# Kernel tuning notes

Measured on AMD Instinct MI355X. Metric: run time of the kernel, lower is better.

The kernel has to match this reference:

```python
import jax, jax.numpy as jnp
import numpy as np

# Multi-scale feature pyramid (static: determines per-level slice bounds)
SPATIAL_SHAPES = np.array([[100, 100], [50, 50], [25, 25], [13, 13], [7, 7]])  # (H, W) per level
LEVEL_START = np.concatenate([[0], np.cumsum(SPATIAL_SHAPES[:, 0] * SPATIAL_SHAPES[:, 1])])[:-1]
C = 256       # hidden_inplanes
HEADS = 8     # head_nums
POINTS = 4    # point_nums
LEVELS = 5    # feature_level_nums
FF = 2048     # feedforward_planes
DH = C // HEADS


def setup_inputs() -> dict:
    key = jax.random.key(0)
    ks = jax.random.split(key, 16)
    B = 2
    L = int((SPATIAL_SHAPES[:, 0] * SPATIAL_SHAPES[:, 1]).sum())  # 13343 tokens
    s = 0.02
    return {
        'src': jax.random.normal(ks[0], (B, L, C), jnp.float32),
        'pos': jax.random.normal(ks[1], (B, L, C), jnp.float32) * 0.1,
        'reference_points': jax.random.uniform(ks[2], (B, L, LEVELS, 2), jnp.float32),
        'wv': jax.random.normal(ks[3], (C, C), jnp.float32) * s,
        'bv': jnp.zeros((C,), jnp.float32),
        'wo': jax.random.normal(ks[4], (C, HEADS * LEVELS * POINTS * 2), jnp.float32) * s,
        'bo': jax.random.normal(ks[5], (HEADS * LEVELS * POINTS * 2,), jnp.float32) * 0.5,
        'wa': jax.random.normal(ks[6], (C, HEADS * LEVELS * POINTS), jnp.float32) * s,
        'ba': jnp.zeros((HEADS * LEVELS * POINTS,), jnp.float32),
        'wout': jax.random.normal(ks[7], (C, C), jnp.float32) * s,
        'bout': jnp.zeros((C,), jnp.float32),
        'ln1g': jnp.ones((C,), jnp.float32),
        'ln1b': jnp.zeros((C,), jnp.float32),
        'w1': jax.random.normal(ks[8], (C, FF), jnp.float32) * s,
        'b1': jnp.zeros((FF,), jnp.float32),
        'w2': jax.random.normal(ks[9], (FF, C), jnp.float32) * s,
        'b2': jnp.zeros((C,), jnp.float32),
        'ln2g': jnp.ones((C,), jnp.float32),
        'ln2b': jnp.zeros((C,), jnp.float32),
    }


def layernorm(x, g, b, eps=1e-5):
    m = jnp.mean(x, -1, keepdims=True)
    v = jnp.var(x, -1, keepdims=True)
    return (x - m) * jax.lax.rsqrt(v + eps) * g + b


def bilinear_sample(val, loc, Hs, Ws):
    # val: [B, heads, H*W, dh]   loc: [B, heads, Lq, P, 2] normalized coords in [0,1]
    # grid_sample semantics, align_corners=False, zero padding outside
    px = loc[..., 0] * Ws - 0.5
    py = loc[..., 1] * Hs - 0.5
    x0 = jnp.floor(px); y0 = jnp.floor(py)
    lx = px - x0;       ly = py - y0
    x0i = x0.astype(jnp.int32); y0i = y0.astype(jnp.int32)
    gather = jax.vmap(jax.vmap(lambda v, i: v[i]))  # over batch, head dims
    out = jnp.zeros(loc.shape[:-1] + (val.shape[-1],), val.dtype)
    for dx, dy, w in ((0, 0, (1 - lx) * (1 - ly)), (1, 0, lx * (1 - ly)),
                      (0, 1, (1 - lx) * ly), (1, 1, lx * ly)):
        xi = x0i + dx; yi = y0i + dy
        valid = (xi >= 0) & (xi < Ws) & (yi >= 0) & (yi < Hs)
        idx = jnp.clip(yi, 0, Hs - 1) * Ws + jnp.clip(xi, 0, Ws - 1)
        g = gather(val, idx)  # [B, heads, Lq, P, dh]
        out = out + (w * valid)[..., None] * g
    return out


def msdeform_attn(query, value_in, ref, wv, bv, wo, bo, wa, ba, wout, bout):
    B, Lq, _ = query.shape
    # value projection -> [B, heads, Len, dh]
    value = (value_in @ wv + bv).reshape(B, -1, HEADS, DH).transpose(0, 2, 1, 3)
    offsets = (query @ wo + bo).reshape(B, Lq, HEADS, LEVELS, POINTS, 2)
    attn = jax.nn.softmax((query @ wa + ba).reshape(B, Lq, HEADS, LEVELS * POINTS), -1)
    attn = attn.reshape(B, Lq, HEADS, LEVELS, POINTS)
    # offset normalizer = (W, H) per level
    norml = jnp.asarray(SPATIAL_SHAPES[:, ::-1].copy(), jnp.float32)
    loc = ref[:, :, None, :, None, :] + offsets / norml[None, None, None, :, None, :]
    acc = jnp.zeros((B, Lq, HEADS, DH), query.dtype)
    for l in range(LEVELS):
        Hs, Ws = int(SPATIAL_SHAPES[l, 0]), int(SPATIAL_SHAPES[l, 1])
        s = int(LEVEL_START[l])
        vl = value[:, :, s:s + Hs * Ws, :]
        locl = jnp.transpose(loc[:, :, :, l], (0, 2, 1, 3, 4))  # [B, heads, Lq, P, 2]
        samp = bilinear_sample(vl, locl, Hs, Ws)                 # [B, heads, Lq, P, dh]
        acc = acc + jnp.einsum('bhqpd,bqhp->bqhd', samp, attn[:, :, :, l])
    return acc.reshape(B, Lq, C) @ wout + bout


def reference(src, pos, reference_points, wv, bv, wo, bo, wa, ba, wout, bout,
              ln1g, ln1b, w1, b1, w2, b2, ln2g, ln2b):
    # DeformableTransformerEncoderLayer (eval mode, dropout off)
    q = src + pos
    src2 = msdeform_attn(q, src, reference_points, wv, bv, wo, bo, wa, ba, wout, bout)
    x = layernorm(src + src2, ln1g, ln1b)
    ffn = jax.nn.relu(x @ w1 + b1) @ w2 + b2
    return layernorm(x + ffn, ln2g, ln2b)
```

## Files before the change

kernel.cpp:

```cpp
#include <hip/hip_runtime.h>
#include <hip/hip_bf16.h>
#include <hip/hip_fp16.h>

typedef __hip_bfloat16 bf16;
typedef unsigned short ushort_t;
typedef __attribute__((ext_vector_type(8))) short bf16x8;
typedef __attribute__((ext_vector_type(16))) float f32x16;

__device__ __forceinline__ float us2f(unsigned short u) {
    unsigned int x = ((unsigned int)u) << 16;
    return __uint_as_float(x);
}
__device__ __forceinline__ ushort_t f2us(float f) {
    return ((__hip_bfloat16_raw)__float2bfloat16(f)).x;
}

__device__ __forceinline__ void gl_lds16(const ushort_t* g, ushort_t* l) {
    __builtin_amdgcn_global_load_lds(
        (const __attribute__((address_space(1))) void*)g,
        (__attribute__((address_space(3))) void*)l, 16, 0, 0);
}

__global__ __launch_bounds__(256) void cast2_kernel(
    const float* __restrict__ src, const float* __restrict__ pos,
    bf16* __restrict__ src_b, bf16* __restrict__ q_b, int n)
{
    int i = (blockIdx.x * 256 + threadIdx.x) * 4;
    if (i < n) {
        const float4 s4 = *reinterpret_cast<const float4*>(&src[i]);
        const float4 p4 = *reinterpret_cast<const float4*>(&pos[i]);
        int2 sp, qp;
        sp.x = (unsigned)f2us(s4.x) | ((unsigned)f2us(s4.y) << 16);
        sp.y = (unsigned)f2us(s4.z) | ((unsigned)f2us(s4.w) << 16);
        qp.x = (unsigned)f2us(s4.x + p4.x) | ((unsigned)f2us(s4.y + p4.y) << 16);
        qp.y = (unsigned)f2us(s4.z + p4.z) | ((unsigned)f2us(s4.w + p4.w) << 16);
        *reinterpret_cast<int2*>((ushort_t*)src_b + i) = sp;
        *reinterpret_cast<int2*>((ushort_t*)q_b + i) = qp;
    }
}

__global__ __launch_bounds__(256) void prep_kernel(
    const float* __restrict__ wv, const float* __restrict__ wo,
    const float* __restrict__ wa, const float* __restrict__ wout,
    const float* __restrict__ w1, const float* __restrict__ w2,
    const float* __restrict__ bo, const float* __restrict__ ba,
    bf16* __restrict__ wvt, bf16* __restrict__ wcat, bf16* __restrict__ woutt,
    bf16* __restrict__ w1t, bf16* __restrict__ w2t, float* __restrict__ bcat)
{
    __shared__ float tile[32][33];
    const int b = blockIdx.x;
    const float* W; bf16* Wt; int K, N, tb;
    if (b < 64)        { W = wv;   Wt = wvt;            K = 256;  N = 256;  tb = b; }
    else if (b < 144)  { W = wo;   Wt = wcat;           K = 256;  N = 320;  tb = b - 64; }
    else if (b < 184)  { W = wa;   Wt = wcat + 320*256; K = 256;  N = 160;  tb = b - 144; }
    else if (b < 248)  { W = wout; Wt = woutt;          K = 256;  N = 256;  tb = b - 184; }
    else if (b < 760)  { W = w1;   Wt = w1t;            K = 256;  N = 2048; tb = b - 248; }
    else if (b < 1272) { W = w2;   Wt = w2t;            K = 2048; N = 256;  tb = b - 760; }
    else {
        int i = (b - 1272) * 256 + threadIdx.x;
        if (i < 320) bcat[i] = bo[i];
        else if (i < 480) bcat[i] = ba[i - 320];
        return;
    }
    const int ntn = N >> 5;
    const int nb = (tb % ntn) * 32, kb = (tb / ntn) * 32;
    const int tx = threadIdx.x & 31, ty = threadIdx.x >> 5;
    #pragma unroll
    for (int i = 0; i < 32; i += 8) {
        int k = kb + ty + i, n = nb + tx;
        tile[ty + i][tx] = (k < K && n < N) ? W[(size_t)k * N + n] : 0.f;
    }
    __syncthreads();
    #pragma unroll
    for (int i = 0; i < 32; i += 8) {
        int n = nb + ty + i, k = kb + tx;
        if (n < N && k < K)
            Wt[(size_t)n * K + k] = __float2bfloat16(tile[tx][ty + i]);
    }
}

template<bool RELU, bool OUT_BF16, bool HAS_RESID, bool RESID_BF16, int NT, int WPE>
__global__ __launch_bounds__(256, WPE) void gemm_mfma_s(
    const ushort_t* __restrict__ A,
    const ushort_t* __restrict__ Bt,
    const float* __restrict__ bias,
    const void* __restrict__ residv,
    void* __restrict__ outv, int M, int N, int K, int mtiles)
{
    __shared__ __align__(16) char smemraw[24576];
    ushort_t* Asmem = (ushort_t*)smemraw;
    ushort_t* Bsmem = (ushort_t*)(smemraw + 4096);
    float (*epi)[68] = (float(*)[68])smemraw;

    const int lid = blockIdx.x;
    const int tbk = lid >> 3;
    const int xb = tbk & (NT - 1);
    const int yg = (tbk / NT) * 8 + (lid & 7);
    if (yg >= mtiles) return;
    const int m0 = yg * 64;
    const int n0 = xb * 128;

    const int tid = threadIdx.x;
    const int lane = tid & 63;
    const int wave = tid >> 6;
    const int l32 = lane & 31;
    const int hi  = lane >> 5;
    const int wm = wave >> 1;
    const int wn = wave & 1;

    const int lsup = lane >> 3;
    const int clin = lane & 7;

    const int gsA = wave * 8 + lsup;
    const int csA = clin ^ (gsA & 7);
    int rA = m0 + gsA * 2 + (csA >> 2); if (rA > M - 1) rA = M - 1;
    const ushort_t* aP = A + (size_t)rA * K + (csA & 3) * 8;
    ushort_t* aL = Asmem + wave * 512;

    const ushort_t* bP[2]; ushort_t* bL[2];
    #pragma unroll
    for (int i = 0; i < 2; ++i) {
        const int gsB = wave * 16 + i * 8 + lsup;
        const int csB = clin ^ (gsB & 7);
        int rB = n0 + gsB * 2 + (csB >> 2); if (rB > N - 1) rB = N - 1;
        bP[i] = Bt + (size_t)rB * K + (csB & 3) * 8;
        bL[i] = Bsmem + (wave * 16 + i * 8) * 64;
    }

    const int arow = wm * 32 + l32;
    const int asup = arow >> 1;
    const ushort_t* aR[2];
    #pragma unroll
    for (int kw = 0; kw < 2; ++kw) {
        const int q = kw * 2 + hi;
        const int slot = (((arow & 1) << 2) | q) ^ (asup & 7);
        aR[kw] = Asmem + asup * 64 + slot * 8;
    }
    const ushort_t* bR[2][2];
    #pragma unroll
    for (int j = 0; j < 2; ++j) {
        const int brow = wn * 64 + j * 32 + l32;
        const int bsup = brow >> 1;
        #pragma unroll
        for (int kw = 0; kw < 2; ++kw) {
            const int q = kw * 2 + hi;
            const int slot = (((brow & 1) << 2) | q) ^ (bsup & 7);
            bR[j][kw] = Bsmem + bsup * 64 + slot * 8;
        }
    }

    f32x16 acc[2] = {};

    auto stage = [&](int ofs) {
        gl_lds16(aP, aL + ofs);             aP    += 32;
        gl_lds16(bP[0], bL[0] + ofs);       bP[0] += 32;
        gl_lds16(bP[1], bL[1] + ofs);       bP[1] += 32;
    };
    auto compute = [&](int ofs) {
        #pragma unroll
        for (int kw = 0; kw < 2; ++kw) {
            const bf16x8 af = *reinterpret_cast<const bf16x8*>(aR[kw] + ofs);
            #pragma unroll
            for (int j = 0; j < 2; ++j)
                acc[j] = __builtin_amdgcn_mfma_f32_32x32x16_bf16(
                    af, *reinterpret_cast<const bf16x8*>(bR[j][kw] + ofs),
                    acc[j], 0, 0, 0);
        }
    };

    const int ntile = K >> 5;
    stage(0);
    for (int t = 0; t < ntile; t += 2) {
        __syncthreads();
        stage(6144);
        compute(0);
        __syncthreads();
        if (t + 2 < ntile) stage(0);
        compute(6144);
    }
    __syncthreads();

    #pragma unroll
    for (int half = 0; half < 2; ++half) {
        if (wn == half) {
            #pragma unroll
            for (int j = 0; j < 2; ++j) {
                const int coll = j * 32 + l32;
                const int n = n0 + half * 64 + coll;
                const float bv = (n < N) ? bias[n] : 0.f;
                #pragma unroll
                for (int r = 0; r < 16; ++r) {
                    const int row = wm * 32 + hi * 4 + (r & 3) + (r >> 2) * 8;
                    epi[row][coll] = acc[j][r] + bv;
                }
            }
        }
        __syncthreads();
        #pragma unroll
        for (int i = 0; i < 4; ++i) {
            const int idx = i * 256 + tid;
            const int row = idx >> 4;
            const int c4  = idx & 15;
            const int m = m0 + row;
            const int n = n0 + half * 64 + c4 * 4;
            if (m < M && n + 3 < N) {
                float4 v = *reinterpret_cast<const float4*>(&epi[row][c4 * 4]);
                if (HAS_RESID) {
                    if (RESID_BF16) {
                        const int2 rw = *reinterpret_cast<const int2*>(
                            (const ushort_t*)residv + (size_t)m * N + n);
                        v.x += us2f((ushort_t)((unsigned)rw.x & 0xffffu));
                        v.y += us2f((ushort_t)((unsigned)rw.x >> 16));
                        v.z += us2f((ushort_t)((unsigned)rw.y & 0xffffu));
                        v.w += us2f((ushort_t)((unsigned)rw.y >> 16));
                    } else {
                        const float4 r4 = *reinterpret_cast<const float4*>(
                            (const float*)residv + (size_t)m * N + n);
                        v.x += r4.x; v.y += r4.y; v.z += r4.z; v.w += r4.w;
                    }
                }
                if (RELU) {
                    v.x = fmaxf(v.x, 0.f); v.y = fmaxf(v.y, 0.f);
                    v.z = fmaxf(v.z, 0.f); v.w = fmaxf(v.w, 0.f);
                }
                if (OUT_BF16) {
                    int2 pk;
                    pk.x = (unsigned)f2us(v.x) | ((unsigned)f2us(v.y) << 16);
                    pk.y = (unsigned)f2us(v.z) | ((unsigned)f2us(v.w) << 16);
                    *reinterpret_cast<int2*>((ushort_t*)outv + (size_t)m * N + n) = pk;
                } else {
                    *reinterpret_cast<float4*>((float*)outv + (size_t)m * N + n) = v;
                }
            }
        }
        if (half == 0) __syncthreads();
    }
}

__global__ __launch_bounds__(256) void msda_kernel_v7(
    const ushort_t* __restrict__ og,
    const float* __restrict__ refp,
    const ushort_t* __restrict__ value,
    bf16* __restrict__ out,
    int M, int L)
{
    const int tid = threadIdx.x;
    const int nb = gridDim.x;
    int wk = blockIdx.x;
    if ((nb & 7) == 0) {
        const int per = nb >> 3;
        wk = (blockIdx.x & 7) * per + (blockIdx.x >> 3);
    }
    const int qbase = wk * 8;

    __shared__ float s_attn[8][160];
    __shared__ int2  s_off[1280];
    __shared__ int2  s_wh[1280];

    for (int i = tid; i < 1280; i += 256) {
        int q = i / 160, j = i - q * 160;
        int qq = qbase + q;
        s_attn[q][j] = (qq < M) ? us2f(og[(size_t)qq * 480 + 320 + j]) : 0.f;
    }
    __syncthreads();

    if (tid < 64) {
        float* a = &s_attn[tid >> 3][(tid & 7) * 20];
        float mx = -1e30f;
        #pragma unroll
        for (int i = 0; i < 20; ++i) mx = fmaxf(mx, a[i]);
        float ssum = 0.f;
        #pragma unroll
        for (int i = 0; i < 20; ++i) {
            float e = __expf(a[i] - mx);
            a[i] = e;
            ssum += e;
        }
        float inv = 1.f / ssum;
        #pragma unroll
        for (int i = 0; i < 20; ++i) a[i] *= inv;
    }
    __syncthreads();

    #pragma unroll
    for (int it = 0; it < 5; ++it) {
        const int t = tid + it * 256;
        const int q  = t / 160;
        const int r  = t - q * 160;
        const int l  = (r - (r / 20) * 20) >> 2;
        const int qq = qbase + q;

        int2 offp = {0, 0};
        __half2 h01 = __floats2half2_rn(0.f, 0.f);
        __half2 h23 = h01;
        if (qq < M) {
            const int Wi = (l == 0) ? 100 : (l == 1) ? 50 : (l == 2) ? 25
                         : (l == 3) ? 13 : 7;
            const int s0 = (l == 0) ? 0 : (l == 1) ? 10000 : (l == 2) ? 12500
                         : (l == 3) ? 13125 : 13294;
            const float Wf = (float)Wi;
            const float ox = us2f(og[(size_t)qq * 480 + r * 2]);
            const float oy = us2f(og[(size_t)qq * 480 + r * 2 + 1]);
            const float2 rf = *reinterpret_cast<const float2*>(
                &refp[(size_t)qq * 10 + l * 2]);
            const float a = s_attn[q][r];

            const float px = fmaf(rf.x, Wf, -0.5f) + ox;
            const float py = fmaf(rf.y, Wf, -0.5f) + oy;
            const float x0f = floorf(px);
            const float y0f = floorf(py);
            const float lx = px - x0f;
            const float ly = py - y0f;
            const int x0 = (int)x0f;
            const int y0 = (int)y0f;

            const float wx0v = (x0 >= 0 && x0 < Wi) ? (1.f - lx) : 0.f;
            const float wx1v = (x0 + 1 >= 0 && x0 + 1 < Wi) ? lx : 0.f;
            const float wy0v = (y0 >= 0 && y0 < Wi) ? (1.f - ly) : 0.f;
            const float wy1v = (y0 + 1 >= 0 && y0 + 1 < Wi) ? ly : 0.f;

            const int c0 = min(max(x0, 0), Wi - 2);
            const int r0 = min(max(y0, 0), Wi - 2);
            const float swx0 = (x0 == c0 ? wx0v : 0.f) + (x0 + 1 == c0 ? wx1v : 0.f);
            const float swx1 = (x0 == c0 + 1 ? wx0v : 0.f) + (x0 + 1 == c0 + 1 ? wx1v : 0.f);
            const float swy0 = (y0 == r0 ? wy0v : 0.f) + (y0 + 1 == r0 ? wy1v : 0.f);
            const float swy1 = (y0 == r0 + 1 ? wy0v : 0.f) + (y0 + 1 == r0 + 1 ? wy1v : 0.f);

            offp.x = (s0 + r0 * Wi + c0) * 512;
            offp.y = offp.x + Wi * 512;
            h01 = __floats2half2_rn(a * swx0 * swy0, a * swx1 * swy0);
            h23 = __floats2half2_rn(a * swx0 * swy1, a * swx1 * swy1);
        }
        s_off[t] = offp;
        union { __half2 h; int i; } c0u, c1u;
        c0u.h = h01; c1u.h = h23;
        int2 wpk; wpk.x = c0u.i; wpk.y = c1u.i;
        s_wh[t] = wpk;
    }
    __syncthreads();

    const int qi  = tid >> 5;
    const int g   = tid & 31;
    const int h   = g >> 2;
    const int sub = g & 3;
    const int bq = qbase + qi;
    if (bq >= M) return;
    const int b = bq / L;

    const char* vb = (const char*)value + (size_t)b * L * 512 + h * 64 + sub * 16;

    float acc[8] = {};
    const int tb = qi * 160 + h * 20;
    #pragma unroll 2
    for (int p = 0; p < 20; ++p) {
        const int2 off = s_off[tb + p];
        const int2 whp = s_wh[tb + p];
        const int4 u00 = *reinterpret_cast<const int4*>(vb + off.x);
        const int4 u10 = *reinterpret_cast<const int4*>(vb + off.x + 512);
        const int4 u01 = *reinterpret_cast<const int4*>(vb + off.y);
        const int4 u11 = *reinterpret_cast<const int4*>(vb + off.y + 512);
        union { int i; __half2 h; } w0u, w1u;
        w0u.i = whp.x; w1u.i = whp.y;
        const float2 w01 = __half22float2(w0u.h);
        const float2 w23 = __half22float2(w1u.h);
        #define ACC4(u, wt)                                                        \
            acc[0] = fmaf(wt, __uint_as_float((unsigned)(u).x << 16), acc[0]);      \
            acc[1] = fmaf(wt, __uint_as_float((unsigned)(u).x & 0xffff0000u), acc[1]); \
            acc[2] = fmaf(wt, __uint_as_float((unsigned)(u).y << 16), acc[2]);      \
            acc[3] = fmaf(wt, __uint_as_float((unsigned)(u).y & 0xffff0000u), acc[3]); \
            acc[4] = fmaf(wt, __uint_as_float((unsigned)(u).z << 16), acc[4]);      \
            acc[5] = fmaf(wt, __uint_as_float((unsigned)(u).z & 0xffff0000u), acc[5]); \
            acc[6] = fmaf(wt, __uint_as_float((unsigned)(u).w << 16), acc[6]);      \
            acc[7] = fmaf(wt, __uint_as_float((unsigned)(u).w & 0xffff0000u), acc[7]);
        ACC4(u00, w01.x)
        ACC4(u10, w01.y)
        ACC4(u01, w23.x)
        ACC4(u11, w23.y)
        #undef ACC4
    }

    ushort_t o[8];
    #pragma unroll
    for (int i = 0; i < 8; ++i) o[i] = f2us(acc[i]);
    int4 pkt;
    pkt.x = (int)o[0] | ((int)o[1] << 16);
    pkt.y = (int)o[2] | ((int)o[3] << 16);
    pkt.z = (int)o[4] | ((int)o[5] << 16);
    pkt.w = (int)o[6] | ((int)o[7] << 16);
    *reinterpret_cast<int4*>((ushort_t*)out + (size_t)bq * 256 + h * 32 + sub * 8) = pkt;
}

template<bool OUT_BF16>
__global__ __launch_bounds__(256) void ln_kernel(
    const ushort_t* __restrict__ yb, const float* __restrict__ g,
    const float* __restrict__ bta, void* __restrict__ outv, int M)
{
    const int wave = threadIdx.x >> 6, lane = threadIdx.x & 63;
    const int row = blockIdx.x * 4 + wave;
    if (row >= M) return;
    const int2 raw = *reinterpret_cast<const int2*>(&yb[(size_t)row * 256 + lane * 4]);
    float v0 = us2f((ushort_t)((unsigned)raw.x & 0xffffu));
    float v1 = us2f((ushort_t)((unsigned)raw.x >> 16));
    float v2 = us2f((ushort_t)((unsigned)raw.y & 0xffffu));
    float v3 = us2f((ushort_t)((unsigned)raw.y >> 16));
    float s  = v0 + v1 + v2 + v3;
    float ss = v0 * v0 + v1 * v1 + v2 * v2 + v3 * v3;
    #pragma unroll
    for (int o = 32; o > 0; o >>= 1) {
        s += __shfl_down(s, o);
        ss += __shfl_down(ss, o);
    }
    s = __shfl(s, 0);
    ss = __shfl(ss, 0);
    const float mean = s * (1.f / 256.f);
    const float var = ss * (1.f / 256.f) - mean * mean;
    const float rs = rsqrtf(var + 1e-5f);
    const float4 g4 = *reinterpret_cast<const float4*>(&g[lane * 4]);
    const float4 b4 = *reinterpret_cast<const float4*>(&bta[lane * 4]);
    float4 o4;
    o4.x = (v0 - mean) * rs * g4.x + b4.x;
    o4.y = (v1 - mean) * rs * g4.y + b4.y;
    o4.z = (v2 - mean) * rs * g4.z + b4.z;
    o4.w = (v3 - mean) * rs * g4.w + b4.w;
    if (OUT_BF16) {
        int2 pk;
        pk.x = (unsigned)f2us(o4.x) | ((unsigned)f2us(o4.y) << 16);
        pk.y = (unsigned)f2us(o4.z) | ((unsigned)f2us(o4.w) << 16);
        *reinterpret_cast<int2*>((ushort_t*)outv + (size_t)row * 256 + lane * 4) = pk;
    } else {
        *reinterpret_cast<float4*>((float*)outv + (size_t)row * 256 + lane * 4) = o4;
    }
}

extern "C" void kernel_launch(void* const* d_in, const int* in_sizes, int n_in,
                              void* d_out, int out_size, void* d_ws, size_t ws_size,
                              hipStream_t stream)
{
    const int B = 2, L = 13343, C = 256, FF = 2048;
    const int M = B * L;

    const float* src  = (const float*)d_in[0];
    const float* pos  = (const float*)d_in[1];
    const float* refp = (const float*)d_in[2];
    const float* wv   = (const float*)d_in[3];
    const float* bv   = (const float*)d_in[4];
    const float* wo   = (const float*)d_in[5];
    const float* bo   = (const float*)d_in[6];
    const float* wa   = (const float*)d_in[7];
    const float* ba   = (const float*)d_in[8];
    const float* wout = (const float*)d_in[9];
    const float* bout = (const float*)d_in[10];
    const float* ln1g = (const float*)d_in[11];
    const float* ln1b = (const float*)d_in[12];
    const float* w1   = (const float*)d_in[13];
    const float* b1   = (const float*)d_in[14];
    const float* w2   = (const float*)d_in[15];
    const float* b2   = (const float*)d_in[16];
    const float* ln2g = (const float*)d_in[17];
    const float* ln2b = (const float*)d_in[18];

    char* ws = (char*)d_ws;
    const size_t MB = 1ull << 20;
    bf16*  src_b  = (bf16*)(ws + 0);
    bf16*  q_b    = (bf16*)(ws + 14 * MB);
    bf16*  val_b  = (bf16*)(ws + 28 * MB);
    bf16*  og     = (bf16*)(ws + 42 * MB);
    bf16*  acc_b  = (bf16*)(ws + 95 * MB);
    bf16*  h_b    = (bf16*)(ws + 0);
    bf16*  y      = (bf16*)(ws + 110 * MB);
    bf16*  z      = (bf16*)(ws + 110 * MB);
    bf16*  x_b    = (bf16*)(ws + 138 * MB);
    bf16* wvt    = (bf16*)(ws + 152 * MB);
    bf16* wcat   = wvt + 256 * 256;
    bf16* woutt  = wcat + 480 * 256;
    bf16* w1t    = woutt + 256 * 256;
    bf16* w2t    = w1t + 2048 * 256;
    float* bcat  = (float*)(w2t + 256 * 2048);
    (void)ws_size; (void)n_in; (void)in_sizes; (void)out_size;

    const int mt64 = (M + 63) / 64;
    const int gm8  = (mt64 + 7) / 8;
    const int lnb  = (M + 3) / 4;

    prep_kernel<<<1274, 256, 0, stream>>>(wv, wo, wa, wout, w1, w2, bo, ba,
                                          wvt, wcat, woutt, w1t, w2t, bcat);

    cast2_kernel<<<(M * C / 4 + 255) / 256, 256, 0, stream>>>(
        src, pos, src_b, q_b, M * C);

    gemm_mfma_s<false, true, false, false, 2, 4><<<gm8 * 16, 256, 0, stream>>>(
        (const ushort_t*)src_b, (const ushort_t*)wvt, bv, nullptr, val_b,
        M, 256, 256, mt64);

    gemm_mfma_s<false, true, false, false, 4, 4><<<gm8 * 32, 256, 0, stream>>>(
        (const ushort_t*)q_b, (const ushort_t*)wcat, bcat, nullptr, og,
        M, 480, 256, mt64);

    msda_kernel_v7<<<(M + 7) / 8, 256, 0, stream>>>(
        (const ushort_t*)og, refp, (const ushort_t*)val_b, acc_b, M, L);

    gemm_mfma_s<false, true, true, false, 2, 4><<<gm8 * 16, 256, 0, stream>>>(
        (const ushort_t*)acc_b, (const ushort_t*)woutt, bout, src, y,
        M, 256, 256, mt64);

    ln_kernel<true><<<lnb, 256, 0, stream>>>(
        (const ushort_t*)y, ln1g, ln1b, x_b, M);

    gemm_mfma_s<true, true, false, false, 16, 4><<<gm8 * 128, 256, 0, stream>>>(
        (const ushort_t*)x_b, (const ushort_t*)w1t, b1, nullptr, h_b,
        M, FF, 256, mt64);

    gemm_mfma_s<false, true, true, true, 2, 4><<<gm8 * 16, 256, 0, stream>>>(
        (const ushort_t*)h_b, (const ushort_t*)w2t, b2, x_b, z,
        M, 256, FF, mt64);

    ln_kernel<false><<<lnb, 256, 0, stream>>>(
        (const ushort_t*)z, ln2g, ln2b, (float*)d_out, M);
}
```

Measured before the change: 354.0 us.

## Add 128x128-tile MFMA GEMM and use it for projection and FFN GEMMs

Adds a new GEMM kernel with 128x128 output tiles, where each wave computes a 64x64 block from four 32x32x16 bf16 MFMAs. It double-buffers K-slices in LDS through direct global-to-LDS loads with an XOR swizzle, and writes the epilogue through an LDS staging buffer in quadrants. The offset/attention projection GEMM and both FFN GEMMs now use this kernel instead of the 64-row-tile kernel. The goal is more operand reuse per LDS load and higher arithmetic intensity. In exchange there are fewer blocks (grid tail effects), more register pressure, and extra syncs in the epilogue.

```diff
diff --git a/kernel.cpp b/kernel.cpp
--- a/kernel.cpp
+++ b/kernel.cpp
@@ -234,6 +234,173 @@
             }
         }
         if (half == 0) __syncthreads();
+    }
+}
+
+template<bool RELU, bool OUT_BF16, bool HAS_RESID, bool RESID_BF16, int NT>
+__global__ __launch_bounds__(256, 4) void gemm_mfma_b(
+    const ushort_t* __restrict__ A,
+    const ushort_t* __restrict__ Bt,
+    const float* __restrict__ bias,
+    const void* __restrict__ residv,
+    void* __restrict__ outv, int M, int N, int K, int mtiles)
+{
+    __shared__ __align__(16) char smemraw[32768];
+    ushort_t* Asmem = (ushort_t*)smemraw;
+    ushort_t* Bsmem = (ushort_t*)(smemraw + 8192);
+    float (*epi)[68] = (float(*)[68])smemraw;
+
+    const int lid = blockIdx.x;
+    const int tbk = lid >> 3;
+    const int xb = tbk & (NT - 1);
+    const int yg = (tbk / NT) * 8 + (lid & 7);
+    if (yg >= mtiles) return;
+    const int m0 = yg * 128;
+    const int n0 = xb * 128;
+
+    const int tid = threadIdx.x;
+    const int lane = tid & 63;
+    const int wave = tid >> 6;
+    const int l32 = lane & 31;
+    const int hi  = lane >> 5;
+    const int wm = wave >> 1;
+    const int wn = wave & 1;
+
+    const int lsup = lane >> 3;
+    const int clin = lane & 7;
+    const ushort_t *aP[2], *bP[2];
+    ushort_t *aL[2], *bL[2];
+    #pragma unroll
+    for (int i = 0; i < 2; ++i) {
+        const int gs = wave * 16 + i * 8 + lsup;
+        const int cs = clin ^ (gs & 7);
+        int rA = m0 + gs * 2 + (cs >> 2); if (rA > M - 1) rA = M - 1;
+        aP[i] = A + (size_t)rA * K + (cs & 3) * 8;
+        aL[i] = Asmem + (wave * 16 + i * 8) * 64;
+        int rB = n0 + gs * 2 + (cs >> 2); if (rB > N - 1) rB = N - 1;
+        bP[i] = Bt + (size_t)rB * K + (cs & 3) * 8;
+        bL[i] = Bsmem + (wave * 16 + i * 8) * 64;
+    }
+
+    const ushort_t* aR[2][2];
+    const ushort_t* bR[2][2];
+    #pragma unroll
+    for (int mi = 0; mi < 2; ++mi) {
+        const int arow = wm * 64 + mi * 32 + l32;
+        const int asup = arow >> 1;
+        #pragma unroll
+        for (int kw = 0; kw < 2; ++kw) {
+            const int q = kw * 2 + hi;
+            const int slot = (((arow & 1) << 2) | q) ^ (asup & 7);
+            aR[mi][kw] = Asmem + asup * 64 + slot * 8;
+        }
+    }
+    #pragma unroll
+    for (int ni = 0; ni < 2; ++ni) {
+        const int brow = wn * 64 + ni * 32 + l32;
+        const int bsup = brow >> 1;
+        #pragma unroll
+        for (int kw = 0; kw < 2; ++kw) {
+            const int q = kw * 2 + hi;
+            const int slot = (((brow & 1) << 2) | q) ^ (bsup & 7);
+            bR[ni][kw] = Bsmem + bsup * 64 + slot * 8;
+        }
+    }
+
+    f32x16 a00 = {}, a01 = {}, a10 = {}, a11 = {};
+
+    auto stage = [&](int ofs) {
+        gl_lds16(aP[0], aL[0] + ofs); aP[0] += 32;
+        gl_lds16(aP[1], aL[1] + ofs); aP[1] += 32;
+        gl_lds16(bP[0], bL[0] + ofs); bP[0] += 32;
+        gl_lds16(bP[1], bL[1] + ofs); bP[1] += 32;
+    };
+    auto compute = [&](int ofs) {
+        #pragma unroll
+        for (int kw = 0; kw < 2; ++kw) {
+            const bf16x8 af0 = *reinterpret_cast<const bf16x8*>(aR[0][kw] + ofs);
+            const bf16x8 af1 = *reinterpret_cast<const bf16x8*>(aR[1][kw] + ofs);
+            const bf16x8 bf0 = *reinterpret_cast<const bf16x8*>(bR[0][kw] + ofs);
+            const bf16x8 bf1 = *reinterpret_cast<const bf16x8*>(bR[1][kw] + ofs);
+            a00 = __builtin_amdgcn_mfma_f32_32x32x16_bf16(af0, bf0, a00, 0, 0, 0);
+            a01 = __builtin_amdgcn_mfma_f32_32x32x16_bf16(af0, bf1, a01, 0, 0, 0);
+            a10 = __builtin_amdgcn_mfma_f32_32x32x16_bf16(af1, bf0, a10, 0, 0, 0);
+            a11 = __builtin_amdgcn_mfma_f32_32x32x16_bf16(af1, bf1, a11, 0, 0, 0);
+        }
+    };
+
+    const int ntile = K >> 5;
+    stage(0);
+    for (int t = 0; t < ntile; t += 2) {
+        __syncthreads();
+        stage(8192);
+        compute(0);
+        __syncthreads();
+        if (t + 2 < ntile) stage(0);
+        compute(8192);
+    }
+    __syncthreads();
+
+    #pragma unroll
+    for (int qd = 0; qd < 4; ++qd) {
+        const int rh = qd >> 1, ch = qd & 1;
+        if (qd) __syncthreads();
+        if (wm == rh && wn == ch) {
+            #pragma unroll
+            for (int ni = 0; ni < 2; ++ni) {
+                const int col = ni * 32 + l32;
+                const int n = n0 + ch * 64 + col;
+                const float bv = (n < N) ? bias[n] : 0.f;
+                #pragma unroll
+                for (int mi = 0; mi < 2; ++mi) {
+                    const f32x16& ac = (mi == 0) ? (ni == 0 ? a00 : a01)
+                                                 : (ni == 0 ? a10 : a11);
+                    #pragma unroll
+                    for (int r = 0; r < 16; ++r) {
+                        const int row = mi * 32 + hi * 4 + (r & 3) + (r >> 2) * 8;
+                        epi[row][col] = ac[r] + bv;
+                    }
+                }
+            }
+        }
+        __syncthreads();
+        #pragma unroll
+        for (int i = 0; i < 4; ++i) {
+            const int idx = i * 256 + tid;
+            const int row = idx >> 4;
+            const int c4  = idx & 15;
+            const int m = m0 + rh * 64 + row;
+            const int n = n0 + ch * 64 + c4 * 4;
+            if (m < M && n + 3 < N) {
+                float4 v = *reinterpret_cast<const float4*>(&epi[row][c4 * 4]);
+                if (HAS_RESID) {
+                    if (RESID_BF16) {
+                        const int2 rw = *reinterpret_cast<const int2*>(
+                            (const ushort_t*)residv + (size_t)m * N + n);
+                        v.x += us2f((ushort_t)((unsigned)rw.x & 0xffffu));
+                        v.y += us2f((ushort_t)((unsigned)rw.x >> 16));
+                        v.z += us2f((ushort_t)((unsigned)rw.y & 0xffffu));
+                        v.w += us2f((ushort_t)((unsigned)rw.y >> 16));
+                    } else {
+                        const float4 r4 = *reinterpret_cast<const float4*>(
+                            (const float*)residv + (size_t)m * N + n);
+                        v.x += r4.x; v.y += r4.y; v.z += r4.z; v.w += r4.w;
+                    }
+                }
+                if (RELU) {
+                    v.x = fmaxf(v.x, 0.f); v.y = fmaxf(v.y, 0.f);
+                    v.z = fmaxf(v.z, 0.f); v.w = fmaxf(v.w, 0.f);
+                }
+                if (OUT_BF16) {
+                    int2 pk;
+                    pk.x = (unsigned)f2us(v.x) | ((unsigned)f2us(v.y) << 16);
+                    pk.y = (unsigned)f2us(v.z) | ((unsigned)f2us(v.w) << 16);
+                    *reinterpret_cast<int2*>((ushort_t*)outv + (size_t)m * N + n) = pk;
+                } else {
+                    *reinterpret_cast<float4*>((float*)outv + (size_t)m * N + n) = v;
+                }
+            }
+        }
     }
 }
 
@@ -478,9 +645,11 @@
     float* bcat  = (float*)(w2t + 256 * 2048);
     (void)ws_size; (void)n_in; (void)in_sizes; (void)out_size;
 
-    const int mt64 = (M + 63) / 64;
-    const int gm8  = (mt64 + 7) / 8;
-    const int lnb  = (M + 3) / 4;
+    const int mt64  = (M + 63) / 64;
+    const int gm8   = (mt64 + 7) / 8;
+    const int mt128 = (M + 127) / 128;
+    const int gb8   = (mt128 + 7) / 8;
+    const int lnb   = (M + 3) / 4;
 
     prep_kernel<<<1274, 256, 0, stream>>>(wv, wo, wa, wout, w1, w2, bo, ba,
                                           wvt, wcat, woutt, w1t, w2t, bcat);
@@ -492,9 +661,9 @@
         (const ushort_t*)src_b, (const ushort_t*)wvt, bv, nullptr, val_b,
         M, 256, 256, mt64);
 
-    gemm_mfma_s<false, true, false, false, 4, 4><<<gm8 * 32, 256, 0, stream>>>(
+    gemm_mfma_b<false, true, false, false, 4><<<gb8 * 32, 256, 0, stream>>>(
         (const ushort_t*)q_b, (const ushort_t*)wcat, bcat, nullptr, og,
-        M, 480, 256, mt64);
+        M, 480, 256, mt128);
 
     msda_kernel_v7<<<(M + 7) / 8, 256, 0, stream>>>(
         (const ushort_t*)og, refp, (const ushort_t*)val_b, acc_b, M, L);
@@ -506,13 +675,13 @@
     ln_kernel<true><<<lnb, 256, 0, stream>>>(
         (const ushort_t*)y, ln1g, ln1b, x_b, M);
 
-    gemm_mfma_s<true, true, false, false, 16, 4><<<gm8 * 128, 256, 0, stream>>>(
+    gemm_mfma_b<true, true, false, false, 16><<<gb8 * 128, 256, 0, stream>>>(
         (const ushort_t*)x_b, (const ushort_t*)w1t, b1, nullptr, h_b,
-        M, FF, 256, mt64);
-
-    gemm_mfma_s<false, true, true, true, 2, 4><<<gm8 * 16, 256, 0, stream>>>(
+        M, FF, 256, mt128);
+
+    gemm_mfma_b<false, true, true, true, 2><<<gb8 * 16, 256, 0, stream>>>(
         (const ushort_t*)h_b, (const ushort_t*)w2t, b2, x_b, z,
-        M, 256, FF, mt64);
+        M, 256, FF, mt128);
 
     ln_kernel<false><<<lnb, 256, 0, stream>>>(
         (const ushort_t*)z, ln2g, ln2b, (float*)d_out, M);
```

After: 353.6 us. No clear change (-0.1%).
